# Kernel tuning notes

Measured on AMD Instinct MI355X. Metric: run time of the kernel, lower is better.

## Reference

```python
import jax, jax.numpy as jnp
import numpy as np


def setup_inputs() -> dict:
    key = jax.random.key(0)
    ks = jax.random.split(key, 6)
    Bsz, Ch, N, L = 16, 1024, 16, 4096
    return {
        "input": jax.random.normal(ks[0], (Bsz, Ch, L), jnp.float32),
        "A": jax.random.normal(ks[1], (Ch, N, 2), jnp.float32),
        "B": jax.random.normal(ks[2], (Ch, N), jnp.float32),  # unused in 'dws' mode
        "C": jax.random.normal(ks[3], (Ch, N), jnp.float32),  # unused in 'dws' mode
        "log_dt": jax.random.normal(ks[4], (Ch, N), jnp.float32) * 0.5 - 4.0,
        "E": jax.random.normal(ks[5], (Ch, N), jnp.float32),
    }


def reference(input, A, B, C, log_dt, E):
    """Kernelizer forward, mode='dws', run_mode='training'.

    discretize (simplified ZOH):
      A_real = -softplus(A[...,0]); A_imag = A[...,1]; dt = exp(log_dt)
      E_hat = E * dt; dtA = dt * (A_real + i*A_imag)        # (Ch, N)
    kernel: k[c, l] = Re( sum_n E_hat[c,n] * exp(dtA[c,n] * l) )
    output: causal depthwise conv of input with k via 2L-padded FFT.
    """
    L = input.shape[-1]
    A_real = -jax.nn.softplus(A[..., 0])                     # (Ch, N)
    A_imag = A[..., 1]                                       # (Ch, N)
    dt = jnp.exp(log_dt)                                     # (Ch, N)
    E_hat = E * dt                                           # (Ch, N)
    dtA_real = dt * A_real
    dtA_imag = dt * A_imag

    l = jnp.arange(L, dtype=input.dtype)                     # (L,)
    # real part of the complex vandermonde, fused: exp(ar*l) * cos(ai*l)
    vand = jnp.exp(dtA_real[:, :, None] * l) * jnp.cos(dtA_imag[:, :, None] * l)  # (Ch, N, L)
    k = jnp.einsum('cn,cnl->cl', E_hat, vand)                # (Ch, L)

    n_fft = 2 * L  # zero-pad so circular conv == linear causal conv
    Uf = jnp.fft.rfft(input, n=n_fft)                        # (B, Ch, L+1)
    Kf = jnp.fft.rfft(k, n=n_fft)                            # (Ch, L+1)
    y = jnp.fft.irfft(Uf * Kf, n=n_fft)[..., :L]             # (B, Ch, L)
    return y.astype(input.dtype)
```

## Files before the change

### kernel.cpp

```cpp
#include <hip/hip_runtime.h>
#include <hip/hip_bf16.h>

#define CH   1024
#define BSZ  16
#define LSEQ 4096
#define NST  16

typedef __attribute__((ext_vector_type(8))) short short8;
typedef __attribute__((ext_vector_type(4))) float f32x4;

__device__ __forceinline__ unsigned int pkrn(float a, float b) {
    __hip_bfloat162 h = __float22bfloat162_rn(make_float2(a, b));
    unsigned int u;
    __builtin_memcpy(&u, &h, 4);
    return u;
}
__device__ __forceinline__ float rfl(float x) {
    return __int_as_float(__builtin_amdgcn_readfirstlane(__float_as_int(x)));
}
#define DSHR(x, d) __int_as_float(__builtin_amdgcn_update_dpp(0, __float_as_int(x), 0x110 + (d), 0xf, 0xf, true))
#define DBC(x, ctrl, rm) __int_as_float(__builtin_amdgcn_update_dpp(0, __float_as_int(x), (ctrl), (rm), 0xf, true))

#define XT0_OFF 0
#define XT1_OFF 8192
#define S_OFF   16384
#define SIN_OFF 24704
#define SMEM_SZ 28800

__device__ __forceinline__ void barrier_fast() {
    asm volatile("s_waitcnt lgkmcnt(0)\n\ts_barrier" ::: "memory");
}

__global__ __launch_bounds__(256, 4) void conv_k(const float* __restrict__ x,
                                                 const float* __restrict__ A,
                                                 const float* __restrict__ log_dt,
                                                 const float* __restrict__ E,
                                                 float* __restrict__ y) {
    __shared__ __align__(16) char smem[SMEM_SZ];
    const int tid  = threadIdx.x;
    const int w    = tid >> 6, lane = tid & 63;
    const int g    = lane >> 4, l15 = lane & 15;
    const int bid  = blockIdx.x;
    const int c    = bid >> 1;
    const int half = bid & 1;

    const size_t cstride = (size_t)CH * LSEQ;
    const float* xr = x + ((size_t)(8 * half) * CH + c) * (size_t)LSEQ;
    float*       yb = y + ((size_t)(8 * half) * CH + c) * (size_t)LSEQ;

    int stb[2];
#pragma unroll
    for (int it = 0; it < 2; ++it) {
        int slot = it * 256 + tid;
        int m = slot >> 3, js = slot & 7;
        stb[it] = (m * 128 + js * 16) ^ ((m & 7) << 4);
    }
    float4 pend[4];
    auto ldraw = [&](const float* xp) {
#pragma unroll
        for (int it = 0; it < 2; ++it) {
            int slot = it * 256 + tid;
            pend[2 * it]     = *(const float4*)(xp + slot * 8);
            pend[2 * it + 1] = *(const float4*)(xp + slot * 8 + 4);
        }
    };
    auto stage = [&](int xoff) {
#pragma unroll
        for (int it = 0; it < 2; ++it) {
            uint4 pk;
            pk.x = pkrn(pend[2 * it].x,     pend[2 * it].y);
            pk.y = pkrn(pend[2 * it].z,     pend[2 * it].w);
            pk.z = pkrn(pend[2 * it + 1].x, pend[2 * it + 1].y);
            pk.w = pkrn(pend[2 * it + 1].z, pend[2 * it + 1].w);
            *(uint4*)(smem + xoff + stb[it]) = pk;
        }
    };

    ldraw(xr);

    float* PR = (float*)(smem + S_OFF);
    float* PI = PR + NST * 65;
    float* EH = (float*)(smem + SIN_OFF);
    float* KL = EH + NST;
    {
        int n = tid & 15;
        int idx0 = c * NST + n;
        float a0 = A[2 * idx0], a1 = A[2 * idx0 + 1];
        float sp = (a0 > 20.f) ? a0 : log1pf(expf(a0));
        float dtv = expf(log_dt[idx0]);
        float dar = -dtv * sp, dai = dtv * a1;
        if (tid < NST) EH[tid] = E[idx0] * dtv;
        for (int l = tid >> 4; l < 65; l += 16) {
            float mg = expf(dar * (float)l);
            float s, cs;
            sincosf(dai * (float)l, &s, &cs);
            PR[n * 65 + l] = mg * cs;
            PI[n * 65 + l] = mg * s;
        }
    }
    __syncthreads();
    if (tid < 64) {
        float kl = 0.f;
#pragma unroll
        for (int nn = 0; nn < NST; ++nn) kl += EH[nn] * PR[nn * 65 + tid];
        KL[tid] = kl;
    }
    __syncthreads();

    short8 wa[2], pa[3];
    {
        int p = 16 * (w >> 1) + l15;
        const float* tb = ((p & 1) ? PI : PR) + (p >> 1) * 65;
#pragma unroll
        for (int kt = 0; kt < 2; ++kt) {
            union { short8 v; unsigned int d[4]; } u;
#pragma unroll
            for (int e2 = 0; e2 < 4; ++e2) {
                int j = kt * 32 + 8 * g + 2 * e2;
                u.d[e2] = pkrn(tb[63 - j], tb[62 - j]);
            }
            wa[kt] = u.v;
        }
        int i = 16 * w + l15;
#pragma unroll
        for (int kt = 0; kt < 2; ++kt) {
            union { short8 v; unsigned int d[4]; } u;
#pragma unroll
            for (int e2 = 0; e2 < 4; ++e2) {
                int k0 = kt * 32 + 8 * g + 2 * e2;
                float v0 = (k0 <= i)     ? KL[i - k0]     : 0.f;
                float v1 = (k0 + 1 <= i) ? KL[i - k0 - 1] : 0.f;
                u.d[e2] = pkrn(v0, v1);
            }
            pa[kt] = u.v;
        }
        {
            union { short8 v; unsigned int d[4]; } u;
#pragma unroll
            for (int e2 = 0; e2 < 4; ++e2) {
                int n3 = 4 * g + e2;
                float re = EH[n3] * PR[n3 * 65 + i + 1];
                float im = -EH[n3] * PI[n3 * 65 + i + 1];
                u.d[e2] = pkrn(re, im);
            }
            pa[2] = u.v;
        }
    }

    float q1r[4], q1i[4], q2r[4], q2i[4], q4r[4], q4i[4], q8r[4], q8i[4];
    float fr[4], fi[4], hr[4], hi[4];
#pragma unroll
    for (int k = 0; k < 4; ++k) {
        int nn = 4 * w + k;
        float ar = PR[nn * 65 + 64], ai = PI[nn * 65 + 64];
        float b2r = fmaf(ar, ar, -(ai * ai)), b2i = 2.f * ar * ai;
        float b4r = fmaf(b2r, b2r, -(b2i * b2i)), b4i = 2.f * b2r * b2i;
        float b8r = fmaf(b4r, b4r, -(b4i * b4i)), b8i = 2.f * b4r * b4i;
        float b16r = fmaf(b8r, b8r, -(b8i * b8i)), b16i = 2.f * b8r * b8i;
        q1r[k] = rfl(ar);  q1i[k] = rfl(ai);
        q2r[k] = rfl(b2r); q2i[k] = rfl(b2i);
        q4r[k] = rfl(b4r); q4i[k] = rfl(b4i);
        q8r[k] = rfl(b8r); q8i[k] = rfl(b8i);
        float cr = ar, ci = ai;
        {
            float tr = fmaf(cr, ar, -(ci * ai)), ti = fmaf(cr, ai, ci * ar);
            cr = (l15 & 1) ? tr : cr; ci = (l15 & 1) ? ti : ci;
        }
        {
            float tr = fmaf(cr, b2r, -(ci * b2i)), ti = fmaf(cr, b2i, ci * b2r);
            cr = (l15 & 2) ? tr : cr; ci = (l15 & 2) ? ti : ci;
        }
        {
            float tr = fmaf(cr, b4r, -(ci * b4i)), ti = fmaf(cr, b4i, ci * b4r);
            cr = (l15 & 4) ? tr : cr; ci = (l15 & 4) ? ti : ci;
        }
        {
            float tr = fmaf(cr, b8r, -(ci * b8i)), ti = fmaf(cr, b8i, ci * b8r);
            cr = (l15 & 8) ? tr : cr; ci = (l15 & 8) ? ti : ci;
        }
        fr[k] = cr; fi[k] = ci;
        float tr = fmaf(cr, b16r, -(ci * b16i)), ti = fmaf(cr, b16i, ci * b16r);
        bool r3 = (lane >= 48);
        hr[k] = r3 ? tr : cr; hi[k] = r3 ? ti : ci;
    }

    int xfo[4][2], sino[4];
#pragma unroll
    for (int nt = 0; nt < 4; ++nt) {
#pragma unroll
        for (int kt = 0; kt < 2; ++kt)
            xfo[nt][kt] = ((l15 * 128 + kt * 64 + g * 16) ^ ((l15 & 7) << 4)) + nt * 2048;
        sino[nt] = ((l15 * 64 + g * 16) ^ ((l15 & 3) << 4)) + nt * 1024;
    }
    const int ntb  = (w & 1) << 1;
    const int swb  = ((16 * (w >> 1) + 4 * g) * 65 + l15 + 16 * ntb) * 4;
    const int srb  = (8 * w * 65 + lane) * 4;
    const int sinw = (lane * 64 + 16 * w) ^ ((lane & 3) << 4);

    short8 xf[4][2];
    auto rdfrags = [&](int xoff) {
#pragma unroll
        for (int nt = 0; nt < 4; ++nt)
#pragma unroll
            for (int kt = 0; kt < 2; ++kt)
                xf[nt][kt] = *(const short8*)(smem + xoff + xfo[nt][kt]);
    };

    auto gemm1 = [&]() {
        f32x4 a0 = {0.f, 0.f, 0.f, 0.f}, a1 = {0.f, 0.f, 0.f, 0.f};
        if ((w & 1) == 0) {
#pragma unroll
            for (int kt = 0; kt < 2; ++kt) {
                a0 = __builtin_amdgcn_mfma_f32_16x16x32_bf16(wa[kt], xf[0][kt], a0, 0, 0, 0);
                a1 = __builtin_amdgcn_mfma_f32_16x16x32_bf16(wa[kt], xf[1][kt], a1, 0, 0, 0);
            }
        } else {
#pragma unroll
            for (int kt = 0; kt < 2; ++kt) {
                a0 = __builtin_amdgcn_mfma_f32_16x16x32_bf16(wa[kt], xf[2][kt], a0, 0, 0, 0);
                a1 = __builtin_amdgcn_mfma_f32_16x16x32_bf16(wa[kt], xf[3][kt], a1, 0, 0, 0);
            }
        }
#pragma unroll
        for (int r = 0; r < 4; ++r) {
            *(float*)(smem + S_OFF + swb + r * 260)      = a0[r];
            *(float*)(smem + S_OFF + swb + r * 260 + 64) = a1[r];
        }
    };

    auto scan = [&]() {
        float sr[4], si[4];
#pragma unroll
        for (int k = 0; k < 4; ++k) {
            sr[k] = *(const float*)(smem + S_OFF + srb + k * 520);
            si[k] = *(const float*)(smem + S_OFF + srb + k * 520 + 260);
        }
#pragma unroll
        for (int k = 0; k < 4; ++k) {
            { float ur = DSHR(sr[k], 1), ui = DSHR(si[k], 1);
              sr[k] = fmaf(q1r[k], ur, fmaf(-q1i[k], ui, sr[k]));
              si[k] = fmaf(q1r[k], ui, fmaf(q1i[k], ur, si[k])); }
            { float ur = DSHR(sr[k], 2), ui = DSHR(si[k], 2);
              sr[k] = fmaf(q2r[k], ur, fmaf(-q2i[k], ui, sr[k]));
              si[k] = fmaf(q2r[k], ui, fmaf(q2i[k], ur, si[k])); }
            { float ur = DSHR(sr[k], 4), ui = DSHR(si[k], 4);
              sr[k] = fmaf(q4r[k], ur, fmaf(-q4i[k], ui, sr[k]));
              si[k] = fmaf(q4r[k], ui, fmaf(q4i[k], ur, si[k])); }
            { float ur = DSHR(sr[k], 8), ui = DSHR(si[k], 8);
              sr[k] = fmaf(q8r[k], ur, fmaf(-q8i[k], ui, sr[k]));
              si[k] = fmaf(q8r[k], ui, fmaf(q8i[k], ur, si[k])); }
            { float ur = DBC(sr[k], 0x142, 0xa), ui = DBC(si[k], 0x142, 0xa);
              sr[k] = fmaf(fr[k], ur, fmaf(-fi[k], ui, sr[k]));
              si[k] = fmaf(fr[k], ui, fmaf(fi[k], ur, si[k])); }
            { float ur = DBC(sr[k], 0x143, 0xc), ui = DBC(si[k], 0x143, 0xc);
              sr[k] = fmaf(hr[k], ur, fmaf(-hi[k], ui, sr[k]));
              si[k] = fmaf(hr[k], ui, fmaf(hi[k], ur, si[k])); }
        }
        unsigned int dw[4];
#pragma unroll
        for (int k = 0; k < 4; ++k) {
            float ar = __shfl_up(sr[k], 1);
            float ai = __shfl_up(si[k], 1);
            ar = (lane > 0) ? ar : 0.f;
            ai = (lane > 0) ? ai : 0.f;
            dw[k] = pkrn(ar, ai);
        }
        *(uint4*)(smem + SIN_OFF + sinw) = make_uint4(dw[0], dw[1], dw[2], dw[3]);
    };

    auto row = [&](int xc, int xn, float* yr, const float* xpre, bool do_stage) {
        rdfrags(xc);
        gemm1();
        f32x4 acc[4];
#pragma unroll
        for (int nt = 0; nt < 4; ++nt) {
            f32x4 z = {0.f, 0.f, 0.f, 0.f};
            acc[nt] = __builtin_amdgcn_mfma_f32_16x16x32_bf16(pa[0], xf[nt][0], z, 0, 0, 0);
        }
        if (w >= 2) {
#pragma unroll
            for (int nt = 0; nt < 4; ++nt)
                acc[nt] = __builtin_amdgcn_mfma_f32_16x16x32_bf16(pa[1], xf[nt][1], acc[nt], 0, 0, 0);
        }
        asm volatile("" :: "v"(acc[0]), "v"(acc[1]), "v"(acc[2]), "v"(acc[3]));
        if (do_stage) stage(xn);
        if (xpre) ldraw(xpre);
        barrier_fast();
        scan();
        barrier_fast();
#pragma unroll
        for (int nt = 0; nt < 4; ++nt) {
            short8 sf = *(const short8*)(smem + SIN_OFF + sino[nt]);
            acc[nt] = __builtin_amdgcn_mfma_f32_16x16x32_bf16(pa[2], sf, acc[nt], 0, 0, 0);
        }
#pragma unroll
        for (int nt = 0; nt < 4; ++nt) {
            int m = l15 + 16 * nt;
            float4 v = make_float4(acc[nt][0], acc[nt][1], acc[nt][2], acc[nt][3]);
            *(float4*)(yr + m * 64 + 16 * w + 4 * g) = v;
        }
    };

    stage(XT0_OFF);
    ldraw(xr + cstride);
    __syncthreads();

#pragma unroll 1
    for (int bb = 0; bb < 4; ++bb) {
        row(XT0_OFF, XT1_OFF, yb + (size_t)(2 * bb) * cstride,
            (bb < 3) ? (xr + (size_t)(2 * bb + 2) * cstride) : nullptr, true);
        row(XT1_OFF, XT0_OFF, yb + (size_t)(2 * bb + 1) * cstride,
            (bb < 3) ? (xr + (size_t)(2 * bb + 3) * cstride) : nullptr, bb < 3);
    }
}

extern "C" void kernel_launch(void* const* d_in, const int* in_sizes, int n_in,
                              void* d_out, int out_size, void* d_ws, size_t ws_size,
                              hipStream_t stream) {
    const float* x      = (const float*)d_in[0];
    const float* A      = (const float*)d_in[1];
    const float* log_dt = (const float*)d_in[4];
    const float* E      = (const float*)d_in[5];
    float* out = (float*)d_out;
    (void)d_ws; (void)ws_size;

    conv_k<<<2 * CH, 256, 0, stream>>>(x, A, log_dt, E, out);
}
```

Measured before the change: 110.4 us.

## Split fragment loads into halves, shorten prefetch distance, raise occupancy to five

Each wave now loads the X fragments in two halves of two tiles instead of all eight at once, interleaving the scan-input GEMM and the output GEMM on each half, to cut register pressure. The raw-input prefetch distance drops from two rows to one, and staging of the next row moves after the scan. Launch bounds rise from 4 to 5 blocks per SIMD so more blocks can be resident. The trade-off is less latency hiding per block: shared-memory reads are split into two phases and the global prefetch has less time to land before it is staged.

Measured after the change: 152.8 us. 1.38x slower.

```diff
diff --git a/kernel.cpp b/kernel.cpp
--- a/kernel.cpp
+++ b/kernel.cpp
@@ -31,7 +31,7 @@
     asm volatile("s_waitcnt lgkmcnt(0)\n\ts_barrier" ::: "memory");
 }
 
-__global__ __launch_bounds__(256, 4) void conv_k(const float* __restrict__ x,
+__global__ __launch_bounds__(256, 5) void conv_k(const float* __restrict__ x,
                                                  const float* __restrict__ A,
                                                  const float* __restrict__ log_dt,
                                                  const float* __restrict__ E,
@@ -196,37 +196,6 @@
     const int swb  = ((16 * (w >> 1) + 4 * g) * 65 + l15 + 16 * ntb) * 4;
     const int srb  = (8 * w * 65 + lane) * 4;
     const int sinw = (lane * 64 + 16 * w) ^ ((lane & 3) << 4);
-
-    short8 xf[4][2];
-    auto rdfrags = [&](int xoff) {
-#pragma unroll
-        for (int nt = 0; nt < 4; ++nt)
-#pragma unroll
-            for (int kt = 0; kt < 2; ++kt)
-                xf[nt][kt] = *(const short8*)(smem + xoff + xfo[nt][kt]);
-    };
-
-    auto gemm1 = [&]() {
-        f32x4 a0 = {0.f, 0.f, 0.f, 0.f}, a1 = {0.f, 0.f, 0.f, 0.f};
-        if ((w & 1) == 0) {
-#pragma unroll
-            for (int kt = 0; kt < 2; ++kt) {
-                a0 = __builtin_amdgcn_mfma_f32_16x16x32_bf16(wa[kt], xf[0][kt], a0, 0, 0, 0);
-                a1 = __builtin_amdgcn_mfma_f32_16x16x32_bf16(wa[kt], xf[1][kt], a1, 0, 0, 0);
-            }
-        } else {
-#pragma unroll
-            for (int kt = 0; kt < 2; ++kt) {
-                a0 = __builtin_amdgcn_mfma_f32_16x16x32_bf16(wa[kt], xf[2][kt], a0, 0, 0, 0);
-                a1 = __builtin_amdgcn_mfma_f32_16x16x32_bf16(wa[kt], xf[3][kt], a1, 0, 0, 0);
-            }
-        }
-#pragma unroll
-        for (int r = 0; r < 4; ++r) {
-            *(float*)(smem + S_OFF + swb + r * 260)      = a0[r];
-            *(float*)(smem + S_OFF + swb + r * 260 + 64) = a1[r];
-        }
-    };
 
     auto scan = [&]() {
         float sr[4], si[4];
@@ -269,24 +238,77 @@
     };
 
     auto row = [&](int xc, int xn, float* yr, const float* xpre, bool do_stage) {
-        rdfrags(xc);
-        gemm1();
         f32x4 acc[4];
-#pragma unroll
-        for (int nt = 0; nt < 4; ++nt) {
-            f32x4 z = {0.f, 0.f, 0.f, 0.f};
-            acc[nt] = __builtin_amdgcn_mfma_f32_16x16x32_bf16(pa[0], xf[nt][0], z, 0, 0, 0);
-        }
-        if (w >= 2) {
-#pragma unroll
-            for (int nt = 0; nt < 4; ++nt)
-                acc[nt] = __builtin_amdgcn_mfma_f32_16x16x32_bf16(pa[1], xf[nt][1], acc[nt], 0, 0, 0);
+        f32x4 s0 = {0.f, 0.f, 0.f, 0.f}, s1 = {0.f, 0.f, 0.f, 0.f};
+        const f32x4 z = {0.f, 0.f, 0.f, 0.f};
+        short8 xfA[2][2];
+        if ((w & 1) == 0) {
+#pragma unroll
+            for (int kt = 0; kt < 2; ++kt) {
+                xfA[0][kt] = *(const short8*)(smem + xc + xfo[0][kt]);
+                xfA[1][kt] = *(const short8*)(smem + xc + xfo[1][kt]);
+            }
+#pragma unroll
+            for (int kt = 0; kt < 2; ++kt) {
+                s0 = __builtin_amdgcn_mfma_f32_16x16x32_bf16(wa[kt], xfA[0][kt], s0, 0, 0, 0);
+                s1 = __builtin_amdgcn_mfma_f32_16x16x32_bf16(wa[kt], xfA[1][kt], s1, 0, 0, 0);
+            }
+            acc[0] = __builtin_amdgcn_mfma_f32_16x16x32_bf16(pa[0], xfA[0][0], z, 0, 0, 0);
+            acc[1] = __builtin_amdgcn_mfma_f32_16x16x32_bf16(pa[0], xfA[1][0], z, 0, 0, 0);
+            if (w >= 2) {
+                acc[0] = __builtin_amdgcn_mfma_f32_16x16x32_bf16(pa[1], xfA[0][1], acc[0], 0, 0, 0);
+                acc[1] = __builtin_amdgcn_mfma_f32_16x16x32_bf16(pa[1], xfA[1][1], acc[1], 0, 0, 0);
+            }
+#pragma unroll
+            for (int kt = 0; kt < 2; ++kt) {
+                xfA[0][kt] = *(const short8*)(smem + xc + xfo[2][kt]);
+                xfA[1][kt] = *(const short8*)(smem + xc + xfo[3][kt]);
+            }
+            acc[2] = __builtin_amdgcn_mfma_f32_16x16x32_bf16(pa[0], xfA[0][0], z, 0, 0, 0);
+            acc[3] = __builtin_amdgcn_mfma_f32_16x16x32_bf16(pa[0], xfA[1][0], z, 0, 0, 0);
+            if (w >= 2) {
+                acc[2] = __builtin_amdgcn_mfma_f32_16x16x32_bf16(pa[1], xfA[0][1], acc[2], 0, 0, 0);
+                acc[3] = __builtin_amdgcn_mfma_f32_16x16x32_bf16(pa[1], xfA[1][1], acc[3], 0, 0, 0);
+            }
+        } else {
+#pragma unroll
+            for (int kt = 0; kt < 2; ++kt) {
+                xfA[0][kt] = *(const short8*)(smem + xc + xfo[2][kt]);
+                xfA[1][kt] = *(const short8*)(smem + xc + xfo[3][kt]);
+            }
+#pragma unroll
+            for (int kt = 0; kt < 2; ++kt) {
+                s0 = __builtin_amdgcn_mfma_f32_16x16x32_bf16(wa[kt], xfA[0][kt], s0, 0, 0, 0);
+                s1 = __builtin_amdgcn_mfma_f32_16x16x32_bf16(wa[kt], xfA[1][kt], s1, 0, 0, 0);
+            }
+            acc[2] = __builtin_amdgcn_mfma_f32_16x16x32_bf16(pa[0], xfA[0][0], z, 0, 0, 0);
+            acc[3] = __builtin_amdgcn_mfma_f32_16x16x32_bf16(pa[0], xfA[1][0], z, 0, 0, 0);
+            if (w >= 2) {
+                acc[2] = __builtin_amdgcn_mfma_f32_16x16x32_bf16(pa[1], xfA[0][1], acc[2], 0, 0, 0);
+                acc[3] = __builtin_amdgcn_mfma_f32_16x16x32_bf16(pa[1], xfA[1][1], acc[3], 0, 0, 0);
+            }
+#pragma unroll
+            for (int kt = 0; kt < 2; ++kt) {
+                xfA[0][kt] = *(const short8*)(smem + xc + xfo[0][kt]);
+                xfA[1][kt] = *(const short8*)(smem + xc + xfo[1][kt]);
+            }
+            acc[0] = __builtin_amdgcn_mfma_f32_16x16x32_bf16(pa[0], xfA[0][0], z, 0, 0, 0);
+            acc[1] = __builtin_amdgcn_mfma_f32_16x16x32_bf16(pa[0], xfA[1][0], z, 0, 0, 0);
+            if (w >= 2) {
+                acc[0] = __builtin_amdgcn_mfma_f32_16x16x32_bf16(pa[1], xfA[0][1], acc[0], 0, 0, 0);
+                acc[1] = __builtin_amdgcn_mfma_f32_16x16x32_bf16(pa[1], xfA[1][1], acc[1], 0, 0, 0);
+            }
+        }
+#pragma unroll
+        for (int r = 0; r < 4; ++r) {
+            *(float*)(smem + S_OFF + swb + r * 260)      = s0[r];
+            *(float*)(smem + S_OFF + swb + r * 260 + 64) = s1[r];
         }
         asm volatile("" :: "v"(acc[0]), "v"(acc[1]), "v"(acc[2]), "v"(acc[3]));
-        if (do_stage) stage(xn);
         if (xpre) ldraw(xpre);
         barrier_fast();
         scan();
+        if (do_stage) stage(xn);
         barrier_fast();
 #pragma unroll
         for (int nt = 0; nt < 4; ++nt) {
@@ -302,15 +324,14 @@
     };
 
     stage(XT0_OFF);
-    ldraw(xr + cstride);
     __syncthreads();
 
+    int cur = XT0_OFF, nxt = XT1_OFF;
 #pragma unroll 1
-    for (int bb = 0; bb < 4; ++bb) {
-        row(XT0_OFF, XT1_OFF, yb + (size_t)(2 * bb) * cstride,
-            (bb < 3) ? (xr + (size_t)(2 * bb + 2) * cstride) : nullptr, true);
-        row(XT1_OFF, XT0_OFF, yb + (size_t)(2 * bb + 1) * cstride,
-            (bb < 3) ? (xr + (size_t)(2 * bb + 3) * cstride) : nullptr, bb < 3);
+    for (int bb = 0; bb < 8; ++bb) {
+        row(cur, nxt, yb + (size_t)bb * cstride,
+            (bb < 7) ? (xr + (size_t)(bb + 1) * cstride) : nullptr, bb < 7);
+        int t = cur; cur = nxt; nxt = t;
     }
 }
 
```

## Keep chunk-state scan in registers and double-buffer scan output to drop a barrier

Applied to the files above, without the earlier changes.

The old path wrote the chunk-state GEMM results to shared memory, read them back in another layout, scanned, then synced twice per row. Now every wave computes the full state GEMM for its own tiles and scans directly in the MFMA output registers with DPP shifts plus a ds_swizzle cross-tile carry. The scan output is double-buffered, so the final MFMA for a row is deferred into the next iteration and one barrier per row goes away. In exchange each wave does redundant state-GEMM MFMAs (all four tiles instead of two), and the carry path is more intricate.

Result: no change. 110.8 us (+0.3%).

```diff
diff --git a/kernel.cpp b/kernel.cpp
--- a/kernel.cpp
+++ b/kernel.cpp
@@ -2,7 +2,6 @@
 #include <hip/hip_bf16.h>
 
 #define CH   1024
-#define BSZ  16
 #define LSEQ 4096
 #define NST  16
 
@@ -15,17 +14,18 @@
     __builtin_memcpy(&u, &h, 4);
     return u;
 }
-__device__ __forceinline__ float rfl(float x) {
-    return __int_as_float(__builtin_amdgcn_readfirstlane(__float_as_int(x)));
-}
 #define DSHR(x, d) __int_as_float(__builtin_amdgcn_update_dpp(0, __float_as_int(x), 0x110 + (d), 0xf, 0xf, true))
-#define DBC(x, ctrl, rm) __int_as_float(__builtin_amdgcn_update_dpp(0, __float_as_int(x), (ctrl), (rm), 0xf, true))
-
-#define XT0_OFF 0
-#define XT1_OFF 8192
-#define S_OFF   16384
-#define SIN_OFF 24704
-#define SMEM_SZ 28800
+__device__ __forceinline__ float swz15(float x) {
+    return __int_as_float(__builtin_amdgcn_ds_swizzle(__float_as_int(x), 0x1F0));
+}
+
+#define XT0_OFF  0
+#define XT1_OFF  8192
+#define SIN0_OFF 16384
+#define SIN1_OFF 20480
+#define TBL_OFF  16384
+#define EH_OFF   24704
+#define SMEM_SZ  25024
 
 __device__ __forceinline__ void barrier_fast() {
     asm volatile("s_waitcnt lgkmcnt(0)\n\ts_barrier" ::: "memory");
@@ -40,6 +40,7 @@
     const int tid  = threadIdx.x;
     const int w    = tid >> 6, lane = tid & 63;
     const int g    = lane >> 4, l15 = lane & 15;
+    const int a    = w >> 1, s = w & 1;
     const int bid  = blockIdx.x;
     const int c    = bid >> 1;
     const int half = bid & 1;
@@ -78,9 +79,9 @@
 
     ldraw(xr);
 
-    float* PR = (float*)(smem + S_OFF);
+    float* PR = (float*)(smem + TBL_OFF);
     float* PI = PR + NST * 65;
-    float* EH = (float*)(smem + SIN_OFF);
+    float* EH = (float*)(smem + EH_OFF);
     float* KL = EH + NST;
     {
         int n = tid & 15;
@@ -92,10 +93,10 @@
         if (tid < NST) EH[tid] = E[idx0] * dtv;
         for (int l = tid >> 4; l < 65; l += 16) {
             float mg = expf(dar * (float)l);
-            float s, cs;
-            sincosf(dai * (float)l, &s, &cs);
+            float sn, cs;
+            sincosf(dai * (float)l, &sn, &cs);
             PR[n * 65 + l] = mg * cs;
-            PI[n * 65 + l] = mg * s;
+            PI[n * 65 + l] = mg * sn;
         }
     }
     __syncthreads();
@@ -109,7 +110,7 @@
 
     short8 wa[2], pa[3];
     {
-        int p = 16 * (w >> 1) + l15;
+        int p = 16 * a + l15;
         const float* tb = ((p & 1) ? PI : PR) + (p >> 1) * 65;
 #pragma unroll
         for (int kt = 0; kt < 2; ++kt) {
@@ -147,41 +148,24 @@
         }
     }
 
-    float q1r[4], q1i[4], q2r[4], q2i[4], q4r[4], q4i[4], q8r[4], q8i[4];
-    float fr[4], fi[4], hr[4], hi[4];
-#pragma unroll
-    for (int k = 0; k < 4; ++k) {
-        int nn = 4 * w + k;
-        float ar = PR[nn * 65 + 64], ai = PI[nn * 65 + 64];
-        float b2r = fmaf(ar, ar, -(ai * ai)), b2i = 2.f * ar * ai;
-        float b4r = fmaf(b2r, b2r, -(b2i * b2i)), b4i = 2.f * b2r * b2i;
-        float b8r = fmaf(b4r, b4r, -(b4i * b4i)), b8i = 2.f * b4r * b4i;
-        float b16r = fmaf(b8r, b8r, -(b8i * b8i)), b16i = 2.f * b8r * b8i;
-        q1r[k] = rfl(ar);  q1i[k] = rfl(ai);
-        q2r[k] = rfl(b2r); q2i[k] = rfl(b2i);
-        q4r[k] = rfl(b4r); q4i[k] = rfl(b4i);
-        q8r[k] = rfl(b8r); q8i[k] = rfl(b8i);
-        float cr = ar, ci = ai;
-        {
-            float tr = fmaf(cr, ar, -(ci * ai)), ti = fmaf(cr, ai, ci * ar);
-            cr = (l15 & 1) ? tr : cr; ci = (l15 & 1) ? ti : ci;
-        }
-        {
-            float tr = fmaf(cr, b2r, -(ci * b2i)), ti = fmaf(cr, b2i, ci * b2r);
-            cr = (l15 & 2) ? tr : cr; ci = (l15 & 2) ? ti : ci;
-        }
-        {
-            float tr = fmaf(cr, b4r, -(ci * b4i)), ti = fmaf(cr, b4i, ci * b4r);
-            cr = (l15 & 4) ? tr : cr; ci = (l15 & 4) ? ti : ci;
-        }
-        {
-            float tr = fmaf(cr, b8r, -(ci * b8i)), ti = fmaf(cr, b8i, ci * b8r);
-            cr = (l15 & 8) ? tr : cr; ci = (l15 & 8) ? ti : ci;
-        }
-        fr[k] = cr; fi[k] = ci;
-        float tr = fmaf(cr, b16r, -(ci * b16i)), ti = fmaf(cr, b16i, ci * b16r);
-        bool r3 = (lane >= 48);
-        hr[k] = r3 ? tr : cr; hi[k] = r3 ? ti : ci;
+    float q1r, q1i, q2r, q2i, q4r, q4i, q8r, q8i, fr_, fi_;
+    {
+        int nq = 8 * a + 2 * g + s;
+        q1r = PR[nq * 65 + 64];
+        q1i = PI[nq * 65 + 64];
+        q2r = fmaf(q1r, q1r, -(q1i * q1i)); q2i = 2.f * q1r * q1i;
+        q4r = fmaf(q2r, q2r, -(q2i * q2i)); q4i = 2.f * q2r * q2i;
+        q8r = fmaf(q4r, q4r, -(q4i * q4i)); q8i = 2.f * q4r * q4i;
+        float cr = q1r, ci = q1i;
+        { float tr = fmaf(cr, q1r, -(ci * q1i)), ti = fmaf(cr, q1i, ci * q1r);
+          cr = (l15 & 1) ? tr : cr; ci = (l15 & 1) ? ti : ci; }
+        { float tr = fmaf(cr, q2r, -(ci * q2i)), ti = fmaf(cr, q2i, ci * q2r);
+          cr = (l15 & 2) ? tr : cr; ci = (l15 & 2) ? ti : ci; }
+        { float tr = fmaf(cr, q4r, -(ci * q4i)), ti = fmaf(cr, q4i, ci * q4r);
+          cr = (l15 & 4) ? tr : cr; ci = (l15 & 4) ? ti : ci; }
+        { float tr = fmaf(cr, q8r, -(ci * q8i)), ti = fmaf(cr, q8i, ci * q8r);
+          cr = (l15 & 8) ? tr : cr; ci = (l15 & 8) ? ti : ci; }
+        fr_ = cr; fi_ = ci;
     }
 
     int xfo[4][2], sino[4];
@@ -192,105 +176,109 @@
             xfo[nt][kt] = ((l15 * 128 + kt * 64 + g * 16) ^ ((l15 & 7) << 4)) + nt * 2048;
         sino[nt] = ((l15 * 64 + g * 16) ^ ((l15 & 3) << 4)) + nt * 1024;
     }
-    const int ntb  = (w & 1) << 1;
-    const int swb  = ((16 * (w >> 1) + 4 * g) * 65 + l15 + 16 * ntb) * 4;
-    const int srb  = (8 * w * 65 + lane) * 4;
-    const int sinw = (lane * 64 + 16 * w) ^ ((lane & 3) << 4);
-
-    short8 xf[4][2];
-    auto rdfrags = [&](int xoff) {
+    const int sinwb = (l15 * 64 + 8 * g + 32 * a + 4 * s) ^ ((l15 & 3) << 4);
+
+    stage(XT0_OFF);
+    ldraw(xr + cstride);
+    __syncthreads();
+
+    f32x4 acc[4];
+    const f32x4 z = {0.f, 0.f, 0.f, 0.f};
+    int cur = XT0_OFF, nxt = XT1_OFF;
+
+#pragma unroll 1
+    for (int bb = 0; bb < 8; ++bb) {
+        const int sb = (bb & 1) ? SIN1_OFF : SIN0_OFF;
+        if (bb > 0) {
+            const int sbp = (bb & 1) ? SIN0_OFF : SIN1_OFF;
+            float* yr = yb + (size_t)(bb - 1) * cstride;
+#pragma unroll
+            for (int nt = 0; nt < 4; ++nt) {
+                short8 sf = *(const short8*)(smem + sbp + sino[nt]);
+                acc[nt] = __builtin_amdgcn_mfma_f32_16x16x32_bf16(pa[2], sf, acc[nt], 0, 0, 0);
+            }
+#pragma unroll
+            for (int nt = 0; nt < 4; ++nt) {
+                int m = l15 + 16 * nt;
+                float4 v = make_float4(acc[nt][0], acc[nt][1], acc[nt][2], acc[nt][3]);
+                *(float4*)(yr + m * 64 + 16 * w + 4 * g) = v;
+            }
+        }
+
+        short8 xf[4][2];
 #pragma unroll
         for (int nt = 0; nt < 4; ++nt)
 #pragma unroll
             for (int kt = 0; kt < 2; ++kt)
-                xf[nt][kt] = *(const short8*)(smem + xoff + xfo[nt][kt]);
-    };
-
-    auto gemm1 = [&]() {
-        f32x4 a0 = {0.f, 0.f, 0.f, 0.f}, a1 = {0.f, 0.f, 0.f, 0.f};
-        if ((w & 1) == 0) {
-#pragma unroll
-            for (int kt = 0; kt < 2; ++kt) {
-                a0 = __builtin_amdgcn_mfma_f32_16x16x32_bf16(wa[kt], xf[0][kt], a0, 0, 0, 0);
-                a1 = __builtin_amdgcn_mfma_f32_16x16x32_bf16(wa[kt], xf[1][kt], a1, 0, 0, 0);
-            }
-        } else {
-#pragma unroll
-            for (int kt = 0; kt < 2; ++kt) {
-                a0 = __builtin_amdgcn_mfma_f32_16x16x32_bf16(wa[kt], xf[2][kt], a0, 0, 0, 0);
-                a1 = __builtin_amdgcn_mfma_f32_16x16x32_bf16(wa[kt], xf[3][kt], a1, 0, 0, 0);
-            }
-        }
-#pragma unroll
-        for (int r = 0; r < 4; ++r) {
-            *(float*)(smem + S_OFF + swb + r * 260)      = a0[r];
-            *(float*)(smem + S_OFF + swb + r * 260 + 64) = a1[r];
-        }
-    };
-
-    auto scan = [&]() {
-        float sr[4], si[4];
-#pragma unroll
-        for (int k = 0; k < 4; ++k) {
-            sr[k] = *(const float*)(smem + S_OFF + srb + k * 520);
-            si[k] = *(const float*)(smem + S_OFF + srb + k * 520 + 260);
-        }
-#pragma unroll
-        for (int k = 0; k < 4; ++k) {
-            { float ur = DSHR(sr[k], 1), ui = DSHR(si[k], 1);
-              sr[k] = fmaf(q1r[k], ur, fmaf(-q1i[k], ui, sr[k]));
-              si[k] = fmaf(q1r[k], ui, fmaf(q1i[k], ur, si[k])); }
-            { float ur = DSHR(sr[k], 2), ui = DSHR(si[k], 2);
-              sr[k] = fmaf(q2r[k], ur, fmaf(-q2i[k], ui, sr[k]));
-              si[k] = fmaf(q2r[k], ui, fmaf(q2i[k], ur, si[k])); }
-            { float ur = DSHR(sr[k], 4), ui = DSHR(si[k], 4);
-              sr[k] = fmaf(q4r[k], ur, fmaf(-q4i[k], ui, sr[k]));
-              si[k] = fmaf(q4r[k], ui, fmaf(q4i[k], ur, si[k])); }
-            { float ur = DSHR(sr[k], 8), ui = DSHR(si[k], 8);
-              sr[k] = fmaf(q8r[k], ur, fmaf(-q8i[k], ui, sr[k]));
-              si[k] = fmaf(q8r[k], ui, fmaf(q8i[k], ur, si[k])); }
-            { float ur = DBC(sr[k], 0x142, 0xa), ui = DBC(si[k], 0x142, 0xa);
-              sr[k] = fmaf(fr[k], ur, fmaf(-fi[k], ui, sr[k]));
-              si[k] = fmaf(fr[k], ui, fmaf(fi[k], ur, si[k])); }
-            { float ur = DBC(sr[k], 0x143, 0xc), ui = DBC(si[k], 0x143, 0xc);
-              sr[k] = fmaf(hr[k], ur, fmaf(-hi[k], ui, sr[k]));
-              si[k] = fmaf(hr[k], ui, fmaf(hi[k], ur, si[k])); }
-        }
-        unsigned int dw[4];
-#pragma unroll
-        for (int k = 0; k < 4; ++k) {
-            float ar = __shfl_up(sr[k], 1);
-            float ai = __shfl_up(si[k], 1);
-            ar = (lane > 0) ? ar : 0.f;
-            ai = (lane > 0) ? ai : 0.f;
-            dw[k] = pkrn(ar, ai);
-        }
-        *(uint4*)(smem + SIN_OFF + sinw) = make_uint4(dw[0], dw[1], dw[2], dw[3]);
-    };
-
-    auto row = [&](int xc, int xn, float* yr, const float* xpre, bool do_stage) {
-        rdfrags(xc);
-        gemm1();
-        f32x4 acc[4];
-#pragma unroll
-        for (int nt = 0; nt < 4; ++nt) {
-            f32x4 z = {0.f, 0.f, 0.f, 0.f};
+                xf[nt][kt] = *(const short8*)(smem + cur + xfo[nt][kt]);
+
+        f32x4 sa[4];
+#pragma unroll
+        for (int nt = 0; nt < 4; ++nt) {
+            sa[nt] = __builtin_amdgcn_mfma_f32_16x16x32_bf16(wa[0], xf[nt][0], z, 0, 0, 0);
+            sa[nt] = __builtin_amdgcn_mfma_f32_16x16x32_bf16(wa[1], xf[nt][1], sa[nt], 0, 0, 0);
+        }
+#pragma unroll
+        for (int nt = 0; nt < 4; ++nt)
             acc[nt] = __builtin_amdgcn_mfma_f32_16x16x32_bf16(pa[0], xf[nt][0], z, 0, 0, 0);
-        }
         if (w >= 2) {
 #pragma unroll
             for (int nt = 0; nt < 4; ++nt)
                 acc[nt] = __builtin_amdgcn_mfma_f32_16x16x32_bf16(pa[1], xf[nt][1], acc[nt], 0, 0, 0);
         }
-        asm volatile("" :: "v"(acc[0]), "v"(acc[1]), "v"(acc[2]), "v"(acc[3]));
-        if (do_stage) stage(xn);
-        if (xpre) ldraw(xpre);
+
+        float pr[4], pi[4];
+#pragma unroll
+        for (int nt = 0; nt < 4; ++nt) {
+            pr[nt] = s ? sa[nt][2] : sa[nt][0];
+            pi[nt] = s ? sa[nt][3] : sa[nt][1];
+        }
+#pragma unroll
+        for (int nt = 0; nt < 4; ++nt) {
+            { float ur = DSHR(pr[nt], 1), ui = DSHR(pi[nt], 1);
+              pr[nt] = fmaf(q1r, ur, fmaf(-q1i, ui, pr[nt]));
+              pi[nt] = fmaf(q1r, ui, fmaf(q1i, ur, pi[nt])); }
+            { float ur = DSHR(pr[nt], 2), ui = DSHR(pi[nt], 2);
+              pr[nt] = fmaf(q2r, ur, fmaf(-q2i, ui, pr[nt]));
+              pi[nt] = fmaf(q2r, ui, fmaf(q2i, ur, pi[nt])); }
+            { float ur = DSHR(pr[nt], 4), ui = DSHR(pi[nt], 4);
+              pr[nt] = fmaf(q4r, ur, fmaf(-q4i, ui, pr[nt]));
+              pi[nt] = fmaf(q4r, ui, fmaf(q4i, ur, pi[nt])); }
+            { float ur = DSHR(pr[nt], 8), ui = DSHR(pi[nt], 8);
+              pr[nt] = fmaf(q8r, ur, fmaf(-q8i, ui, pr[nt]));
+              pi[nt] = fmaf(q8r, ui, fmaf(q8i, ur, pi[nt])); }
+        }
+        float bR[3], bI[3];
+#pragma unroll
+        for (int nt = 1; nt < 4; ++nt) {
+            bR[nt - 1] = swz15(pr[nt - 1]);
+            bI[nt - 1] = swz15(pi[nt - 1]);
+            pr[nt] = fmaf(fr_, bR[nt - 1], fmaf(-fi_, bI[nt - 1], pr[nt]));
+            pi[nt] = fmaf(fr_, bI[nt - 1], fmaf(fi_, bR[nt - 1], pi[nt]));
+        }
+#pragma unroll
+        for (int nt = 0; nt < 4; ++nt) {
+            float eR = DSHR(pr[nt], 1), eI = DSHR(pi[nt], 1);
+            float b0R = (nt == 0) ? 0.f : bR[nt - 1];
+            float b0I = (nt == 0) ? 0.f : bI[nt - 1];
+            eR = (l15 == 0) ? b0R : eR;
+            eI = (l15 == 0) ? b0I : eI;
+            *(unsigned int*)(smem + sb + sinwb + nt * 1024) = pkrn(eR, eI);
+        }
+
+        if (bb < 7) stage(nxt);
+        if (bb < 6) ldraw(xr + (size_t)(bb + 2) * cstride);
+
         barrier_fast();
-        scan();
-        barrier_fast();
-#pragma unroll
-        for (int nt = 0; nt < 4; ++nt) {
-            short8 sf = *(const short8*)(smem + SIN_OFF + sino[nt]);
+        int t = cur; cur = nxt; nxt = t;
+    }
+
+    {
+        const int sbp = SIN1_OFF;
+        float* yr = yb + (size_t)7 * cstride;
+#pragma unroll
+        for (int nt = 0; nt < 4; ++nt) {
+            short8 sf = *(const short8*)(smem + sbp + sino[nt]);
             acc[nt] = __builtin_amdgcn_mfma_f32_16x16x32_bf16(pa[2], sf, acc[nt], 0, 0, 0);
         }
 #pragma unroll
@@ -299,18 +287,6 @@
             float4 v = make_float4(acc[nt][0], acc[nt][1], acc[nt][2], acc[nt][3]);
             *(float4*)(yr + m * 64 + 16 * w + 4 * g) = v;
         }
-    };
-
-    stage(XT0_OFF);
-    ldraw(xr + cstride);
-    __syncthreads();
-
-#pragma unroll 1
-    for (int bb = 0; bb < 4; ++bb) {
-        row(XT0_OFF, XT1_OFF, yb + (size_t)(2 * bb) * cstride,
-            (bb < 3) ? (xr + (size_t)(2 * bb + 2) * cstride) : nullptr, true);
-        row(XT1_OFF, XT0_OFF, yb + (size_t)(2 * bb + 1) * cstride,
-            (bb < 3) ? (xr + (size_t)(2 * bb + 3) * cstride) : nullptr, bb < 3);
     }
 }
 
```
